# Kernel optimization log

Measured on AMD Instinct MI355X. Metric: run time of the kernel, lower is better.

Reference implementation:

```python
import jax, jax.numpy as jnp
import numpy as np

B, S, N, F = 64, 4096, 25, 3

def setup_inputs() -> dict:
    key = jax.random.key(0)
    x = jax.random.normal(key, (B, S, N, F), dtype=jnp.float32)
    return {"x": x}

def reference(x):
    # x: [B, S, N, F]. For each step i, pair with step i+1 (last step pairs with itself),
    # vectorized as a shift along the seq axis instead of the original Python loops.
    x_next = jnp.concatenate([x[:, 1:], x[:, -1:]], axis=1)  # [B,S,N,F]
    diff = x_next - x
    distances = jnp.sqrt(jnp.sum(diff * diff, axis=-1))  # [B,S,N]
    dot = jnp.sum(x * x_next, axis=-1)
    l2_x = jnp.sqrt(jnp.sum(x * x, axis=-1))
    l2_xn = jnp.sqrt(jnp.sum(x_next * x_next, axis=-1))
    angles = jnp.nan_to_num(jnp.arccos(dot / (l2_x * l2_xn)))  # [B,S,N]
    feats = jnp.stack([distances, angles], axis=-1)  # [B,S,N,2]
    # Original wraps feats in Variable(requires_grad=False): constant w.r.t. grads.
    feats = jax.lax.stop_gradient(feats)
    return jnp.concatenate([x, feats], axis=-1)  # [B,S,N,F+2]
```

## Files before the change

### kernel.cpp

```cpp
#include <hip/hip_runtime.h>


constexpr int Bc = 64, Sc = 4096, Nc = 25;
constexpr int TOTAL_G = Bc * Sc * Nc;

__global__ __launch_bounds__(256) void pe_kernel(const float* __restrict__ x,
                                                 float* __restrict__ out) {
    int g = blockIdx.x * 256 + threadIdx.x;
    if (g >= TOTAL_G) return;

    int row = g / Nc;
    int s = row & (Sc - 1);
    int next_g = (s == Sc - 1) ? g : g + Nc;

    const float* xp = x + 3u * (unsigned)g;
    const float* yp = x + 3u * (unsigned)next_g;
    float x0 = xp[0], x1 = xp[1], x2 = xp[2];
    float y0 = yp[0], y1 = yp[1], y2 = yp[2];

    float d0 = y0 - x0, d1 = y1 - x1, d2 = y2 - x2;
    float dist = sqrtf(d0 * d0 + d1 * d1 + d2 * d2);

    float dot = x0 * y0 + x1 * y1 + x2 * y2;
    float nx = sqrtf(x0 * x0 + x1 * x1 + x2 * x2);
    float ny = sqrtf(y0 * y0 + y1 * y1 + y2 * y2);
    float ratio = dot / (nx * ny);
    float ang = acosf(ratio);
    if (isnan(ang)) ang = 0.0f;

    float* op = out + 5u * (unsigned)g;
    op[0] = x0;
    op[1] = x1;
    op[2] = x2;
    op[3] = dist;
    op[4] = ang;
}

extern "C" void kernel_launch(void* const* d_in, const int* in_sizes, int n_in,
                              void* d_out, int out_size, void* d_ws, size_t ws_size,
                              hipStream_t stream) {
    const float* x = (const float*)d_in[0];
    float* out = (float*)d_out;
    int grid = (TOTAL_G + 255) / 256;
    pe_kernel<<<grid, 256, 0, stream>>>(x, out);
}
```

Baseline: 186.3 us.

## Stage row tiles through shared memory for coalesced float4 loads and stores

Each block loads a tile of 64 sequence rows (plus one halo row) into shared memory using float4 loads, computes the distance and angle features from shared memory, writes the 5-wide output tile into shared memory, then stores it with float4 writes. This replaces strided scalar loads and stride-5 scalar stores that coalesce poorly. It adds about 51 KB of shared memory per block, which limits occupancy, and two barriers per block.

Result: slower. 191.8 us (+2.9%).

```diff
diff --git a/kernel.cpp b/kernel.cpp
--- a/kernel.cpp
+++ b/kernel.cpp
@@ -1,39 +1,63 @@
 #include <hip/hip_runtime.h>
 
 
-constexpr int Bc = 64, Sc = 4096, Nc = 25;
-constexpr int TOTAL_G = Bc * Sc * Nc;
+constexpr int Nc = 25, Sc = 4096, Bc = 64;
+constexpr int TILE_ROWS = 64;
+constexpr int IN_TILE   = TILE_ROWS * 75;
+constexpr int IN_LOAD4  = (IN_TILE + 75 + 3) / 4;
+constexpr int OUT_TILE  = TILE_ROWS * 125;
+constexpr int GROUPS_PER_TILE = TILE_ROWS * Nc;
+constexpr long TOTAL_FLOATS_IN = (long)Bc * Sc * 75;
+constexpr int NUM_TILES = Bc * Sc / TILE_ROWS;
+constexpr int TILES_PER_BATCH = Sc / TILE_ROWS;
 
 __global__ __launch_bounds__(256) void pe_kernel(const float* __restrict__ x,
                                                  float* __restrict__ out) {
-    int g = blockIdx.x * 256 + threadIdx.x;
-    if (g >= TOTAL_G) return;
+    __shared__ float s_in[IN_LOAD4 * 4];
+    __shared__ float s_out[OUT_TILE];
 
-    int row = g / Nc;
-    int s = row & (Sc - 1);
-    int next_g = (s == Sc - 1) ? g : g + Nc;
+    const int tile = blockIdx.x;
+    const long base_in = (long)tile * IN_TILE;
 
-    const float* xp = x + 3u * (unsigned)g;
-    const float* yp = x + 3u * (unsigned)next_g;
-    float x0 = xp[0], x1 = xp[1], x2 = xp[2];
-    float y0 = yp[0], y1 = yp[1], y2 = yp[2];
+    const float4* __restrict__ src4 = (const float4*)(x + base_in);
+    float4* dst4 = (float4*)s_in;
+    for (int i = threadIdx.x; i < IN_LOAD4; i += 256) {
+        if (base_in + (long)i * 4 + 4 <= TOTAL_FLOATS_IN)
+            dst4[i] = src4[i];
+    }
+    __syncthreads();
 
-    float d0 = y0 - x0, d1 = y1 - x1, d2 = y2 - x2;
-    float dist = sqrtf(d0 * d0 + d1 * d1 + d2 * d2);
+    const bool batch_final = ((tile & (TILES_PER_BATCH - 1)) == TILES_PER_BATCH - 1);
+    for (int gl = threadIdx.x; gl < GROUPS_PER_TILE; gl += 256) {
+        int lr = gl / Nc;
+        int off = gl * 3;
+        int noff = (batch_final && lr == TILE_ROWS - 1) ? off : off + 75;
 
-    float dot = x0 * y0 + x1 * y1 + x2 * y2;
-    float nx = sqrtf(x0 * x0 + x1 * x1 + x2 * x2);
-    float ny = sqrtf(y0 * y0 + y1 * y1 + y2 * y2);
-    float ratio = dot / (nx * ny);
-    float ang = acosf(ratio);
-    if (isnan(ang)) ang = 0.0f;
+        float x0 = s_in[off],  x1 = s_in[off + 1],  x2 = s_in[off + 2];
+        float y0 = s_in[noff], y1 = s_in[noff + 1], y2 = s_in[noff + 2];
 
-    float* op = out + 5u * (unsigned)g;
-    op[0] = x0;
-    op[1] = x1;
-    op[2] = x2;
-    op[3] = dist;
-    op[4] = ang;
+        float d0 = y0 - x0, d1 = y1 - x1, d2 = y2 - x2;
+        float dist = sqrtf(d0 * d0 + d1 * d1 + d2 * d2);
+
+        float dot = x0 * y0 + x1 * y1 + x2 * y2;
+        float nx = sqrtf(x0 * x0 + x1 * x1 + x2 * x2);
+        float ny = sqrtf(y0 * y0 + y1 * y1 + y2 * y2);
+        float ang = acosf(dot / (nx * ny));
+        if (isnan(ang)) ang = 0.0f;
+
+        int oo = gl * 5;
+        s_out[oo]     = x0;
+        s_out[oo + 1] = x1;
+        s_out[oo + 2] = x2;
+        s_out[oo + 3] = dist;
+        s_out[oo + 4] = ang;
+    }
+    __syncthreads();
+
+    const float4* so4 = (const float4*)s_out;
+    float4* __restrict__ dstg = (float4*)(out + (long)tile * OUT_TILE);
+    for (int i = threadIdx.x; i < OUT_TILE / 4; i += 256)
+        dstg[i] = so4[i];
 }
 
 extern "C" void kernel_launch(void* const* d_in, const int* in_sizes, int n_in,
@@ -41,6 +65,5 @@
                               hipStream_t stream) {
     const float* x = (const float*)d_in[0];
     float* out = (float*)d_out;
-    int grid = (TOTAL_G + 255) / 256;
-    pe_kernel<<<grid, 256, 0, stream>>>(x, out);
+    pe_kernel<<<NUM_TILES, 256, 0, stream>>>(x, out);
 }
```

## Stage tiles through LDS for coalesced float4 loads and stores, 4 groups per thread

Applied to the files above, without the earlier changes.

Each block loads its contiguous input tile plus a one-row halo into shared memory with float4 loads. Each thread then computes four groups from LDS and writes its 20 outputs back to LDS. The block finally stores them to global memory as coalesced float4 writes. This replaces the strided 3-float loads and 5-float stores of the old per-thread layout, at the cost of extra LDS traffic and three barriers.

Result: slower. 193.4 us (+3.8%).

```diff
diff --git a/kernel.cpp b/kernel.cpp
--- a/kernel.cpp
+++ b/kernel.cpp
@@ -1,39 +1,86 @@
 #include <hip/hip_runtime.h>
 
 
-constexpr int Bc = 64, Sc = 4096, Nc = 25;
-constexpr int TOTAL_G = Bc * Sc * Nc;
+constexpr int Nc = 25, Sc = 4096;
+constexpr int BLOCK = 256;
+constexpr int GPT = 4;
+constexpr int GROUPS_PER_BLOCK = BLOCK * GPT;
+constexpr int IN_FLOATS  = GROUPS_PER_BLOCK * 3 + Nc * 3;
+constexpr int IN_LOAD4   = (IN_FLOATS + 3) / 4;
+constexpr int OUT_FLOATS = GROUPS_PER_BLOCK * 5;
+constexpr long TOTAL_IN  = 64L * Sc * Nc * 3;
+constexpr int NUM_BLOCKS = (int)(64L * Sc * Nc / GROUPS_PER_BLOCK);
 
-__global__ __launch_bounds__(256) void pe_kernel(const float* __restrict__ x,
-                                                 float* __restrict__ out) {
-    int g = blockIdx.x * 256 + threadIdx.x;
-    if (g >= TOTAL_G) return;
+__global__ __launch_bounds__(BLOCK) void pe_kernel(const float* __restrict__ x,
+                                                   float* __restrict__ out) {
+    __shared__ float s_buf[OUT_FLOATS];
 
-    int row = g / Nc;
-    int s = row & (Sc - 1);
-    int next_g = (s == Sc - 1) ? g : g + Nc;
+    const int blk = blockIdx.x;
+    const long base_in = (long)blk * (GROUPS_PER_BLOCK * 3);
 
-    const float* xp = x + 3u * (unsigned)g;
-    const float* yp = x + 3u * (unsigned)next_g;
-    float x0 = xp[0], x1 = xp[1], x2 = xp[2];
-    float y0 = yp[0], y1 = yp[1], y2 = yp[2];
+    {
+        const float4* __restrict__ src4 = (const float4*)(x + base_in);
+        float4* d4 = (float4*)s_buf;
+        #pragma unroll
+        for (int k = 0; k < 4; ++k) {
+            int i = threadIdx.x + k * BLOCK;
+            if (i < IN_LOAD4 && base_in + (long)(i + 1) * 4 <= TOTAL_IN)
+                d4[i] = src4[i];
+        }
+    }
+    __syncthreads();
 
-    float d0 = y0 - x0, d1 = y1 - x1, d2 = y2 - x2;
-    float dist = sqrtf(d0 * d0 + d1 * d1 + d2 * d2);
+    float o[GPT * 5];
+    {
+        const int t = threadIdx.x;
+        const int g0 = blk * GROUPS_PER_BLOCK + GPT * t;
+        const int r0 = g0 / Nc;
+        const int rem0 = g0 - r0 * Nc;
+        const int lbase = 3 * GPT * t;
+        #pragma unroll
+        for (int j = 0; j < GPT; ++j) {
+            int rem = rem0 + j;
+            int row = r0 + (rem >= Nc ? 1 : 0);
+            bool self = ((row & (Sc - 1)) == Sc - 1);
+            int xo = lbase + 3 * j;
+            int yo = self ? xo : xo + Nc * 3;
 
-    float dot = x0 * y0 + x1 * y1 + x2 * y2;
-    float nx = sqrtf(x0 * x0 + x1 * x1 + x2 * x2);
-    float ny = sqrtf(y0 * y0 + y1 * y1 + y2 * y2);
-    float ratio = dot / (nx * ny);
-    float ang = acosf(ratio);
-    if (isnan(ang)) ang = 0.0f;
+            float x0 = s_buf[xo],     x1 = s_buf[xo + 1], x2 = s_buf[xo + 2];
+            float y0 = s_buf[yo],     y1 = s_buf[yo + 1], y2 = s_buf[yo + 2];
 
-    float* op = out + 5u * (unsigned)g;
-    op[0] = x0;
-    op[1] = x1;
-    op[2] = x2;
-    op[3] = dist;
-    op[4] = ang;
+            float d0 = y0 - x0, d1 = y1 - x1, d2 = y2 - x2;
+            float dist = sqrtf(d0 * d0 + d1 * d1 + d2 * d2);
+
+            float dot = x0 * y0 + x1 * y1 + x2 * y2;
+            float nx = sqrtf(x0 * x0 + x1 * x1 + x2 * x2);
+            float ny = sqrtf(y0 * y0 + y1 * y1 + y2 * y2);
+            float ang = acosf(dot / (nx * ny));
+            if (isnan(ang)) ang = 0.0f;
+
+            o[j * 5]     = x0;
+            o[j * 5 + 1] = x1;
+            o[j * 5 + 2] = x2;
+            o[j * 5 + 3] = dist;
+            o[j * 5 + 4] = ang;
+        }
+    }
+    __syncthreads();
+
+    {
+        float4* w4 = (float4*)(s_buf + 20 * threadIdx.x);
+        #pragma unroll
+        for (int k = 0; k < 5; ++k)
+            w4[k] = make_float4(o[k * 4], o[k * 4 + 1], o[k * 4 + 2], o[k * 4 + 3]);
+    }
+    __syncthreads();
+
+    {
+        const float4* s4 = (const float4*)s_buf;
+        float4* __restrict__ dstg = (float4*)(out + (long)blk * OUT_FLOATS);
+        #pragma unroll
+        for (int k = 0; k < 5; ++k)
+            dstg[threadIdx.x + k * BLOCK] = s4[threadIdx.x + k * BLOCK];
+    }
 }
 
 extern "C" void kernel_launch(void* const* d_in, const int* in_sizes, int n_in,
@@ -41,6 +88,5 @@
                               hipStream_t stream) {
     const float* x = (const float*)d_in[0];
     float* out = (float*)d_out;
-    int grid = (TOTAL_G + 255) / 256;
-    pe_kernel<<<grid, 256, 0, stream>>>(x, out);
+    pe_kernel<<<NUM_BLOCKS, BLOCK, 0, stream>>>(x, out);
 }
```
